# Kernel tuning notes

Measured on AMD Instinct MI355X. Metric: run time of the kernel, lower is better.

## Reference

```python
import jax, jax.numpy as jnp
import numpy as np

SEQ_LEN = 1024
BATCH = 1024
TAG = 32
START = TAG - 2  # '[CLS]'
END = TAG - 1    # '[SEP]'
NEG = -10000.0


def setup_inputs() -> dict:
    key = jax.random.key(0)
    k1, k2, k3 = jax.random.split(key, 3)
    feats = jax.random.normal(k1, (SEQ_LEN, BATCH, TAG), dtype=jnp.float32)
    # valid-length mask: 1.0 for t < length, else 0.0 (float, as torch multiplies by it)
    lengths = jax.random.randint(k2, (BATCH,), SEQ_LEN // 2, SEQ_LEN + 1)
    mask = (jnp.arange(SEQ_LEN)[:, None] < lengths[None, :]).astype(jnp.float32)
    # transition parameter with forbidden moves into START and out of END
    transition = jax.random.normal(k3, (TAG, TAG), dtype=jnp.float32)
    transition = transition.at[START, :].set(NEG).at[:, END].set(NEG)
    return {"feats": feats, "mask": mask, "transition": transition}


def reference(feats, mask, transition):
    # feats: (S, B, T), mask: (S, B), transition: (T, T)
    batch, tag = feats.shape[1], feats.shape[2]
    alpha0 = jnp.full((batch, tag), NEG, dtype=feats.dtype).at[:, START].set(0.0)

    def step(alpha, xs):
        feat_t, mask_t = xs  # (B, T), (B,)
        # score[b, next, prev] = alpha[b, prev] + transition[next, prev] + feat_t[b, next]
        score = alpha[:, None, :] + transition[None, :, :] + feat_t[:, :, None]
        new_alpha = jax.nn.logsumexp(score, axis=-1)  # (B, T)
        m = mask_t[:, None]
        return new_alpha * m + alpha * (1.0 - m), None

    alpha, _ = jax.lax.scan(step, alpha0, (feats, mask))
    alpha = alpha + transition[END][None, :]
    return jax.nn.logsumexp(alpha, axis=-1)  # (B,)
```

## Files before the change

### kernel.cpp

```cpp
#include <hip/hip_runtime.h>

#define SEQ   1024
#define BATCH 1024
#define TAG   32
#define START 30
#define ENDT  31
#define PFD   8

__device__ __forceinline__ float rdlane(float v, int j) {
    return __uint_as_float(__builtin_amdgcn_readlane(__float_as_uint(v), j));
}

__device__ __forceinline__ void crf_core(float v, float fval,
                                         const float* __restrict__ e,
                                         float& vn, float& lg) {
    float r[32];
    #pragma unroll
    for (int j = 0; j < 32; ++j) r[j] = rdlane(v, j);
    __builtin_amdgcn_sched_barrier(0);

    float s0 = r[0] * e[0];
    float s1 = r[1] * e[1];
    float s2 = r[2] * e[2];
    float s3 = r[3] * e[3];
    float s4 = r[4] * e[4];
    float s5 = r[5] * e[5];
    float s6 = r[6] * e[6];
    float s7 = r[7] * e[7];
    #pragma unroll
    for (int j = 1; j < 4; ++j) {
        s0 = fmaf(r[8 * j + 0], e[8 * j + 0], s0);
        s1 = fmaf(r[8 * j + 1], e[8 * j + 1], s1);
        s2 = fmaf(r[8 * j + 2], e[8 * j + 2], s2);
        s3 = fmaf(r[8 * j + 3], e[8 * j + 3], s3);
        s4 = fmaf(r[8 * j + 4], e[8 * j + 4], s4);
        s5 = fmaf(r[8 * j + 5], e[8 * j + 5], s5);
        s6 = fmaf(r[8 * j + 6], e[8 * j + 6], s6);
        s7 = fmaf(r[8 * j + 7], e[8 * j + 7], s7);
    }
    float dot = ((s0 + s1) + (s2 + s3)) + ((s4 + s5) + (s6 + s7));

    float c  = fmaxf(r[0], 1e-20f);
    float ef = __expf(fval);
    float rr = __builtin_amdgcn_rcpf(c);
    lg = __logf(c);
    float sc = ef * rr;
    vn = dot * sc;
}

__global__ __attribute__((amdgpu_waves_per_eu(1, 1)))
__launch_bounds__(64, 1) void crf_fwd_kernel(
    const float* __restrict__ feats,
    const float* __restrict__ mask,
    const float* __restrict__ trans,
    float* __restrict__ out)
{
    const int lane = threadIdx.x;
    const int i    = lane & 31;
    const int b    = blockIdx.x;

    float e[32];
    {
        const float4* tr4 = reinterpret_cast<const float4*>(trans + i * TAG);
        #pragma unroll
        for (int c = 0; c < 8; ++c) {
            float4 t = tr4[c];
            e[4 * c + 0] = __expf(t.x);
            e[4 * c + 1] = __expf(t.y);
            e[4 * c + 2] = __expf(t.z);
            e[4 * c + 3] = __expf(t.w);
        }
    }

    const float* fp = feats + (unsigned)(b * TAG + i);
    const float* mk = mask + (unsigned)b;

    float  v  = (i == START) ? 1.0f : 0.0f;
    double mA = 0.0;

    float fb[PFD], mb[PFD];
    #pragma unroll
    for (int p = 0; p < PFD; ++p) {
        fb[p] = fp[(unsigned)p << 15];
        mb[p] = mk[(unsigned)p << 10];
    }

    for (int t = 0; t < SEQ; t += PFD) {
        #pragma unroll
        for (int p = 0; p < PFD; ++p) {
            unsigned mu = __builtin_amdgcn_readfirstlane(__float_as_uint(mb[p]));
            if (mu != 0u) {
                float vn, lg;
                crf_core(v, fb[p], e, vn, lg);
                if (mu == 0x3f800000u) {
                    v = vn;
                    mA += (double)lg;
                } else {
                    float m   = __uint_as_float(mu);
                    float lv  = __logf(fmaxf(v,  1e-37f));
                    float lvn = __logf(fmaxf(vn, 1e-37f));
                    v = v * __expf(m * (lvn - lv));
                    mA += (double)(m * lg);
                }
            }
            int tn = t + PFD + p; tn = (tn < SEQ) ? tn : (SEQ - 1);
            fb[p] = fp[(unsigned)tn << 15];
            mb[p] = mk[(unsigned)tn << 10];
        }
    }

    float z = v * __expf(trans[ENDT * TAG + i]);
    float mx = z;
    #pragma unroll
    for (int k = 16; k >= 1; k >>= 1)
        mx = fmaxf(mx, __shfl_xor(mx, k, 32));
    float ss = z * __builtin_amdgcn_rcpf(mx);
    #pragma unroll
    for (int k = 16; k >= 1; k >>= 1)
        ss += __shfl_xor(ss, k, 32);
    if (lane == 0)
        out[b] = (float)(mA + (double)__logf(mx) + (double)__logf(ss));
}

extern "C" void kernel_launch(void* const* d_in, const int* in_sizes, int n_in,
                              void* d_out, int out_size, void* d_ws, size_t ws_size,
                              hipStream_t stream) {
    const float* feats = (const float*)d_in[0];
    const float* mask  = (const float*)d_in[1];
    const float* trans = (const float*)d_in[2];
    float* out = (float*)d_out;
    crf_fwd_kernel<<<dim3(BATCH), dim3(64), 0, stream>>>(feats, mask, trans, out);
}
```

Measured before the change: 385.1 us.

## Split CRF recurrence into forward and backward halves run by two waves

Each batch element now uses two waves. One runs the forward alpha recurrence over the first half of the sequence, the other runs a backward (transposed-transition) recurrence from the end over the second half, and the two vectors are combined with a dot product at the end. This halves the serial dependency chain per block. A pre-scan of the mask detects fractional values and falls back to the original single-wave path, since the split relies on the mask being binary. It adds a mask pre-pass, shared-memory exchange and two waves per block in exchange for the shorter chain.

```diff
diff --git a/kernel.cpp b/kernel.cpp
--- a/kernel.cpp
+++ b/kernel.cpp
@@ -6,59 +6,58 @@
 #define START 30
 #define ENDT  31
 #define PFD   8
+#define HALF  512
 
 __device__ __forceinline__ float rdlane(float v, int j) {
     return __uint_as_float(__builtin_amdgcn_readlane(__float_as_uint(v), j));
+}
+
+__device__ __forceinline__ void gather_dot(float v, const float* __restrict__ coef,
+                                           float post, float& vn, float& lg) {
+    float r[32];
+    #pragma unroll
+    for (int j = 0; j < 32; ++j) r[j] = rdlane(v, j);
+    __builtin_amdgcn_sched_barrier(0);
+
+    float s0 = r[0] * coef[0];
+    float s1 = r[1] * coef[1];
+    float s2 = r[2] * coef[2];
+    float s3 = r[3] * coef[3];
+    float s4 = r[4] * coef[4];
+    float s5 = r[5] * coef[5];
+    float s6 = r[6] * coef[6];
+    float s7 = r[7] * coef[7];
+    #pragma unroll
+    for (int j = 1; j < 4; ++j) {
+        s0 = fmaf(r[8 * j + 0], coef[8 * j + 0], s0);
+        s1 = fmaf(r[8 * j + 1], coef[8 * j + 1], s1);
+        s2 = fmaf(r[8 * j + 2], coef[8 * j + 2], s2);
+        s3 = fmaf(r[8 * j + 3], coef[8 * j + 3], s3);
+        s4 = fmaf(r[8 * j + 4], coef[8 * j + 4], s4);
+        s5 = fmaf(r[8 * j + 5], coef[8 * j + 5], s5);
+        s6 = fmaf(r[8 * j + 6], coef[8 * j + 6], s6);
+        s7 = fmaf(r[8 * j + 7], coef[8 * j + 7], s7);
+    }
+    float dot = ((s0 + s1) + (s2 + s3)) + ((s4 + s5) + (s6 + s7));
+
+    float c  = fmaxf(r[0], 1e-20f);
+    float rr = __builtin_amdgcn_rcpf(c);
+    lg = __logf(c);
+    float sc = post * rr;
+    vn = dot * sc;
 }
 
 __device__ __forceinline__ void crf_core(float v, float fval,
                                          const float* __restrict__ e,
                                          float& vn, float& lg) {
-    float r[32];
-    #pragma unroll
-    for (int j = 0; j < 32; ++j) r[j] = rdlane(v, j);
-    __builtin_amdgcn_sched_barrier(0);
-
-    float s0 = r[0] * e[0];
-    float s1 = r[1] * e[1];
-    float s2 = r[2] * e[2];
-    float s3 = r[3] * e[3];
-    float s4 = r[4] * e[4];
-    float s5 = r[5] * e[5];
-    float s6 = r[6] * e[6];
-    float s7 = r[7] * e[7];
-    #pragma unroll
-    for (int j = 1; j < 4; ++j) {
-        s0 = fmaf(r[8 * j + 0], e[8 * j + 0], s0);
-        s1 = fmaf(r[8 * j + 1], e[8 * j + 1], s1);
-        s2 = fmaf(r[8 * j + 2], e[8 * j + 2], s2);
-        s3 = fmaf(r[8 * j + 3], e[8 * j + 3], s3);
-        s4 = fmaf(r[8 * j + 4], e[8 * j + 4], s4);
-        s5 = fmaf(r[8 * j + 5], e[8 * j + 5], s5);
-        s6 = fmaf(r[8 * j + 6], e[8 * j + 6], s6);
-        s7 = fmaf(r[8 * j + 7], e[8 * j + 7], s7);
-    }
-    float dot = ((s0 + s1) + (s2 + s3)) + ((s4 + s5) + (s6 + s7));
-
-    float c  = fmaxf(r[0], 1e-20f);
-    float ef = __expf(fval);
-    float rr = __builtin_amdgcn_rcpf(c);
-    lg = __logf(c);
-    float sc = ef * rr;
-    vn = dot * sc;
-}
-
-__global__ __attribute__((amdgpu_waves_per_eu(1, 1)))
-__launch_bounds__(64, 1) void crf_fwd_kernel(
-    const float* __restrict__ feats,
-    const float* __restrict__ mask,
-    const float* __restrict__ trans,
-    float* __restrict__ out)
-{
-    const int lane = threadIdx.x;
-    const int i    = lane & 31;
-    const int b    = blockIdx.x;
-
+    gather_dot(v, e, __expf(fval), vn, lg);
+}
+
+__device__ void slow_path(const float* __restrict__ feats,
+                          const float* __restrict__ mask,
+                          const float* __restrict__ trans,
+                          float* __restrict__ out, int b, int lane) {
+    const int i = lane & 31;
     float e[32];
     {
         const float4* tr4 = reinterpret_cast<const float4*>(trans + i * TAG);
@@ -71,7 +70,6 @@
             e[4 * c + 3] = __expf(t.w);
         }
     }
-
     const float* fp = feats + (unsigned)(b * TAG + i);
     const float* mk = mask + (unsigned)b;
 
@@ -84,14 +82,17 @@
         fb[p] = fp[(unsigned)p << 15];
         mb[p] = mk[(unsigned)p << 10];
     }
-
     for (int t = 0; t < SEQ; t += PFD) {
         #pragma unroll
         for (int p = 0; p < PFD; ++p) {
             unsigned mu = __builtin_amdgcn_readfirstlane(__float_as_uint(mb[p]));
+            float fv = fb[p];
+            int tn = t + PFD + p; tn = (tn < SEQ) ? tn : (SEQ - 1);
+            fb[p] = fp[(unsigned)tn << 15];
+            mb[p] = mk[(unsigned)tn << 10];
             if (mu != 0u) {
                 float vn, lg;
-                crf_core(v, fb[p], e, vn, lg);
+                crf_core(v, fv, e, vn, lg);
                 if (mu == 0x3f800000u) {
                     v = vn;
                     mA += (double)lg;
@@ -103,12 +104,8 @@
                     mA += (double)(m * lg);
                 }
             }
-            int tn = t + PFD + p; tn = (tn < SEQ) ? tn : (SEQ - 1);
-            fb[p] = fp[(unsigned)tn << 15];
-            mb[p] = mk[(unsigned)tn << 10];
-        }
-    }
-
+        }
+    }
     float z = v * __expf(trans[ENDT * TAG + i]);
     float mx = z;
     #pragma unroll
@@ -120,6 +117,134 @@
         ss += __shfl_xor(ss, k, 32);
     if (lane == 0)
         out[b] = (float)(mA + (double)__logf(mx) + (double)__logf(ss));
+}
+
+__global__ __launch_bounds__(128, 2) void crf_fwd_kernel(
+    const float* __restrict__ feats,
+    const float* __restrict__ mask,
+    const float* __restrict__ trans,
+    float* __restrict__ out)
+{
+    const int tid  = threadIdx.x;
+    const int lane = tid & 63;
+    const int w    = tid >> 6;
+    const int i    = lane & 31;
+    const int b    = blockIdx.x;
+
+    __shared__ float  sX[32], sY[32];
+    __shared__ double sM[2];
+    __shared__ int    sFrac;
+
+    if (tid == 0) sFrac = 0;
+    __syncthreads();
+
+    {
+        const int tb = w * HALF;
+        bool bad = false;
+        #pragma unroll
+        for (int k = 0; k < 8; ++k) {
+            float m = mask[(unsigned)((tb + k * 64 + lane) * BATCH + b)];
+            bad |= (m != 0.0f) & (m != 1.0f);
+        }
+        if (__ballot(bad)) sFrac = 1;
+    }
+    __syncthreads();
+
+    if (sFrac) {
+        if (w == 0) slow_path(feats, mask, trans, out, b, lane);
+        return;
+    }
+
+    const float* fp = feats + (unsigned)(b * TAG + i);
+    const float* mk = mask + (unsigned)b;
+
+    if (w == 0) {
+        float e[32];
+        const float4* tr4 = reinterpret_cast<const float4*>(trans + i * TAG);
+        #pragma unroll
+        for (int c = 0; c < 8; ++c) {
+            float4 t = tr4[c];
+            e[4 * c + 0] = __expf(t.x);
+            e[4 * c + 1] = __expf(t.y);
+            e[4 * c + 2] = __expf(t.z);
+            e[4 * c + 3] = __expf(t.w);
+        }
+        float  v  = (i == START) ? 1.0f : 0.0f;
+        double mA = 0.0;
+
+        float fb[PFD], mb[PFD];
+        #pragma unroll
+        for (int p = 0; p < PFD; ++p) {
+            fb[p] = fp[(unsigned)p << 15];
+            mb[p] = mk[(unsigned)p << 10];
+        }
+        for (int t = 0; t < HALF; t += PFD) {
+            #pragma unroll
+            for (int p = 0; p < PFD; ++p) {
+                unsigned mu = __builtin_amdgcn_readfirstlane(__float_as_uint(mb[p]));
+                float fv = fb[p];
+                int tn = t + PFD + p;
+                fb[p] = fp[(unsigned)tn << 15];
+                mb[p] = mk[(unsigned)tn << 10];
+                if (mu != 0u) {
+                    float vn, lg;
+                    gather_dot(v, e, __expf(fv), vn, lg);
+                    v = vn; mA += (double)lg;
+                }
+            }
+        }
+        if (lane < 32) sX[i] = v;
+        if (lane == 0) sM[0] = mA;
+    } else {
+        float eT[32];
+        #pragma unroll
+        for (int c = 0; c < 32; ++c)
+            eT[c] = __expf(trans[c * TAG + i]);
+        float  y  = __expf(trans[ENDT * TAG + i]);
+        double mB = 0.0;
+
+        float fb[PFD], mb[PFD];
+        #pragma unroll
+        for (int p = 0; p < PFD; ++p) {
+            fb[p] = fp[(unsigned)(SEQ - 1 - p) << 15];
+            mb[p] = mk[(unsigned)(SEQ - 1 - p) << 10];
+        }
+        for (int s = 0; s < HALF; s += PFD) {
+            #pragma unroll
+            for (int p = 0; p < PFD; ++p) {
+                unsigned mu = __builtin_amdgcn_readfirstlane(__float_as_uint(mb[p]));
+                float fv = fb[p];
+                int tn = SEQ - 1 - (s + PFD + p);
+                fb[p] = fp[(unsigned)tn << 15];
+                mb[p] = mk[(unsigned)tn << 10];
+                if (mu != 0u) {
+                    float u = y * __expf(fv);
+                    float yn, lg;
+                    gather_dot(u, eT, 1.0f, yn, lg);
+                    y = yn; mB += (double)lg;
+                }
+            }
+        }
+        if (lane < 32) sY[i] = y;
+        if (lane == 0) sM[1] = mB;
+    }
+    __syncthreads();
+
+    if (w == 0) {
+        float z = sX[i] * sY[i];
+        float mx = z;
+        #pragma unroll
+        for (int k = 16; k >= 1; k >>= 1)
+            mx = fmaxf(mx, __shfl_xor(mx, k, 32));
+        mx = fmaxf(mx, 1e-30f);
+        float ss = z * __builtin_amdgcn_rcpf(mx);
+        #pragma unroll
+        for (int k = 16; k >= 1; k >>= 1)
+            ss += __shfl_xor(ss, k, 32);
+        if (lane == 0)
+            out[b] = (float)(sM[0] + sM[1]
+                             + (double)__logf(mx) + (double)__logf(ss));
+    }
 }
 
 extern "C" void kernel_launch(void* const* d_in, const int* in_sizes, int n_in,
@@ -129,5 +254,5 @@
     const float* mask  = (const float*)d_in[1];
     const float* trans = (const float*)d_in[2];
     float* out = (float*)d_out;
-    crf_fwd_kernel<<<dim3(BATCH), dim3(64), 0, stream>>>(feats, mask, trans, out);
-}
+    crf_fwd_kernel<<<dim3(BATCH), dim3(128), 0, stream>>>(feats, mask, trans, out);
+}
```

New measurement: 319.5 us. -17.0%, faster.
